# Kernel tuning notes

Measured on AMD Instinct MI355X. Metric: run time of the kernel, lower is better.

The kernel has to match this reference:

```python
import jax, jax.numpy as jnp
import numpy as np

D_MODEL = 2048
N_HEADS = 16
HEAD_DIM = D_MODEL // N_HEADS  # 128
MAX_T = 2048
ROPE_BASE = 10000.0


def _rope_tables(head_dim, max_t, base):
    inv = 1.0 / (base ** (np.arange(0, head_dim, 2, dtype=np.float32) / head_dim))
    t = np.arange(max_t, dtype=np.float32)
    fr = np.outer(t, inv)  # (T, head_dim//2)
    return jnp.asarray(np.cos(fr)), jnp.asarray(np.sin(fr))


def setup_inputs() -> dict:
    key = jax.random.key(0)
    k1, k2, k3 = jax.random.split(key, 3)
    B, T = 2, 2048
    x = jax.random.normal(k1, (B, T, D_MODEL), dtype=jnp.float32)
    Wqkv = jax.random.normal(k2, (3 * D_MODEL, D_MODEL), dtype=jnp.float32) * 0.02
    Wout = jax.random.normal(k3, (D_MODEL, D_MODEL), dtype=jnp.float32) * 0.02
    cos, sin = _rope_tables(HEAD_DIM, MAX_T, ROPE_BASE)
    rope_mask = jnp.arange(N_HEADS) < (N_HEADS // 2)  # first 8 heads RoPE, rest NoPE
    return {"x": x, "Wqkv": Wqkv, "Wout": Wout, "cos": cos, "sin": sin, "rope_mask": rope_mask}


def _apply_rope(t, cos, sin):
    # t: (B,H,T,hd); pairs are consecutive elements (x0,x1),(x2,x3),...
    B, H, T, hd = t.shape
    tr = t.reshape(B, H, T, hd // 2, 2)
    c = cos[:T][None, None, :, :]
    s = sin[:T][None, None, :, :]
    re = tr[..., 0] * c - tr[..., 1] * s
    im = tr[..., 0] * s + tr[..., 1] * c
    return jnp.stack([re, im], axis=-1).reshape(B, H, T, hd)


def reference(x, Wqkv, Wout, cos, sin, rope_mask):
    B, T, D = x.shape
    H = rope_mask.shape[0]
    hd = D // H
    qkv = x @ Wqkv.T  # (B,T,3D)
    q, k, v = jnp.split(qkv, 3, axis=-1)
    def heads(a):
        return a.reshape(B, T, H, hd).transpose(0, 2, 1, 3)  # (B,H,T,hd)
    q, k, v = heads(q), heads(k), heads(v)
    m = rope_mask[None, :, None, None]  # broadcast over (B,H,T,hd)
    q = jnp.where(m, _apply_rope(q, cos, sin), q)
    k = jnp.where(m, _apply_rope(k, cos, sin), k)
    scale = 1.0 / jnp.sqrt(jnp.asarray(hd, dtype=q.dtype))
    scores = jnp.einsum('bhtd,bhsd->bhts', q, k) * scale
    causal = jnp.tril(jnp.ones((T, T), dtype=bool))
    scores = jnp.where(causal[None, None], scores, jnp.asarray(-jnp.inf, dtype=scores.dtype))
    p = jax.nn.softmax(scores, axis=-1)
    out = jnp.einsum('bhts,bhsd->bhtd', p, v)
    out = out.transpose(0, 2, 1, 3).reshape(B, T, D)
    return out @ Wout.T
```

## Files before the change

### kernel.cpp

```cpp
#include <hip/hip_runtime.h>
#include <stdint.h>

typedef unsigned short u16;
typedef __attribute__((ext_vector_type(8))) short short8;
typedef __attribute__((ext_vector_type(4))) short s16x4;
typedef __attribute__((ext_vector_type(4))) float f32x4;

__device__ __forceinline__ u16 f2bf(float f) {
  uint32_t x = __float_as_uint(f);
  x += 0x7fff + ((x >> 16) & 1);
  return (u16)(x >> 16);
}
__device__ __forceinline__ float bf2f(u16 u) {
  return __uint_as_float(((uint32_t)u) << 16);
}
__device__ __forceinline__ f32x4 mfma16(short8 a, short8 b, f32x4 c) {
  return __builtin_amdgcn_mfma_f32_16x16x32_bf16(a, b, c, 0, 0, 0);
}
__device__ __forceinline__ f32x4 mfma16k16(s16x4 a, s16x4 b, f32x4 c) {
  return __builtin_amdgcn_mfma_f32_16x16x16bf16_1k(a, b, c, 0, 0, 0);
}
__device__ __forceinline__ void gld16(const u16* g, u16* l) {
  __builtin_amdgcn_global_load_lds(
      (const __attribute__((address_space(1))) unsigned int*)g,
      (__attribute__((address_space(3))) unsigned int*)l, 16, 0, 0);
}
__device__ __forceinline__ float exp2a(float x) {
  float r;
  asm("v_exp_f32 %0, %1" : "=v"(r) : "v"(x));
  return r;
}

__global__ __launch_bounds__(256) void cvt_all(const float* __restrict__ x,
                                               const float* __restrict__ wqkv,
                                               const float* __restrict__ wout,
                                               u16* __restrict__ xb,
                                               u16* __restrict__ wqkvb,
                                               u16* __restrict__ woutb) {
  long i = ((long)blockIdx.x * 256 + threadIdx.x) * 8;
  const float* s;
  u16* d;
  long off;
  if (i < 8388608) {
    s = x; d = xb; off = i;
  } else if (i < 20971520) {
    s = wqkv; d = wqkvb; off = i - 8388608;
  } else {
    s = wout; d = woutb; off = i - 20971520;
  }
  f32x4 a = *(const f32x4*)(s + off);
  f32x4 b = *(const f32x4*)(s + off + 4);
  short8 o;
#pragma unroll
  for (int j = 0; j < 4; j++) {
    o[j] = (short)f2bf(a[j]);
    o[j + 4] = (short)f2bf(b[j]);
  }
  *(short8*)(d + off) = o;
}

template <int EPI>
__global__ __launch_bounds__(256) void gemm_bt(const u16* __restrict__ A,
                                               const u16* __restrict__ B,
                                               int K, void* __restrict__ Cv, int N) {
  __shared__ __align__(16) u16 As[4096];
  __shared__ __align__(16) u16 Bs[4096];
  const int m0 = blockIdx.y * 128, n0 = blockIdx.x * 128;
  const int t = threadIdx.x, w = t >> 6, lane = t & 63;
  const int quad = lane >> 4, l15 = lane & 15;
  const int rb = (w >> 1) * 64, cb = (w & 1) * 64;
  f32x4 acc[4][4] = {};
  const u16* ag = A + (size_t)(m0 + w * 16 + (lane >> 2)) * K + (lane & 3) * 8;
  const u16* bg = B + (size_t)(n0 + w * 16 + (lane >> 2)) * K + (lane & 3) * 8;
  u16* al = As + w * 512 + lane * 8;
  u16* bl = Bs + w * 512 + lane * 8;
  const size_t rowskip = (size_t)64 * K;
  for (int k0 = 0; k0 < K; k0 += 32) {
    __syncthreads();
    gld16(ag, al);
    gld16(ag + rowskip, al + 2048);
    gld16(bg, bl);
    gld16(bg + rowskip, bl + 2048);
    ag += 32;
    bg += 32;
    __syncthreads();
    short8 af[4], bfr[4];
#pragma unroll
    for (int mf = 0; mf < 4; mf++)
      af[mf] = *(const short8*)&As[(rb + mf * 16 + l15) * 32 + quad * 8];
#pragma unroll
    for (int nf = 0; nf < 4; nf++)
      bfr[nf] = *(const short8*)&Bs[(cb + nf * 16 + l15) * 32 + quad * 8];
#pragma unroll
    for (int mf = 0; mf < 4; mf++)
#pragma unroll
      for (int nf = 0; nf < 4; nf++)
        acc[mf][nf] = mfma16(af[mf], bfr[nf], acc[mf][nf]);
  }
  if (EPI == 0) {
    u16* q3 = (u16*)Cv;
    const int which = n0 >> 11;
    if (which == 2) {
#pragma unroll
      for (int mf = 0; mf < 4; mf++)
#pragma unroll
        for (int nf = 0; nf < 4; nf++) {
          int m = m0 + rb + mf * 16 + quad * 4;
          int n = n0 + cb + nf * 16 + l15;
          int dd = n & 2047, hh = dd >> 7, di = dd & 127;
          int bb = m >> 11, tt = m & 2047;
          s16x4 st;
#pragma unroll
          for (int rg = 0; rg < 4; rg++) st[rg] = (short)f2bf(acc[mf][nf][rg]);
          *(s16x4*)(q3 + 16777216 + ((size_t)(bb * 16 + hh) * 128 + di) * 2048 + tt) = st;
        }
    } else {
      const float sc = (which == 0) ? 0.1275174f : 1.0f;
      u16* base = q3 + (size_t)which * 8388608;
#pragma unroll
      for (int mf = 0; mf < 4; mf++)
#pragma unroll
        for (int nf = 0; nf < 4; nf++) {
          int m = m0 + rb + mf * 16 + quad * 4;
          int n = n0 + cb + nf * 16 + l15;
          int dd = n & 2047, hh = dd >> 7, di = dd & 127;
          int bb = m >> 11, tt = m & 2047;
#pragma unroll
          for (int rg = 0; rg < 4; rg++)
            base[((size_t)(bb * 16 + hh) * 2048 + tt + rg) * 128 + di] =
                f2bf(acc[mf][nf][rg] * sc);
        }
    }
  } else {
    float* C = (float*)Cv;
#pragma unroll
    for (int mf = 0; mf < 4; mf++)
#pragma unroll
      for (int nf = 0; nf < 4; nf++)
#pragma unroll
        for (int rg = 0; rg < 4; rg++) {
          int m = m0 + rb + mf * 16 + quad * 4 + rg;
          int n = n0 + cb + nf * 16 + l15;
          C[(size_t)m * N + n] = acc[mf][nf][rg];
        }
  }
}

__global__ __launch_bounds__(256) void rope_k(u16* __restrict__ q, u16* __restrict__ k,
                                              const float* __restrict__ cosT,
                                              const float* __restrict__ sinT) {
  int t = threadIdx.x;
  int row = blockIdx.x * 4 + (t >> 6);
  int i = t & 63;
  int b = row >> 14;
  int h = (row >> 11) & 7;
  int tp = row & 2047;
  size_t base = ((size_t)((b * 16 + h) * 2048 + tp)) * 128 + 2 * i;
  float c = cosT[tp * 64 + i], s = sinT[tp * 64 + i];
  {
    uint32_t u = *(uint32_t*)(q + base);
    float x0 = bf2f((u16)(u & 0xffff)), x1 = bf2f((u16)(u >> 16));
    float re = x0 * c - x1 * s, im = x0 * s + x1 * c;
    *(uint32_t*)(q + base) = (uint32_t)f2bf(re) | ((uint32_t)f2bf(im) << 16);
  }
  {
    uint32_t u = *(uint32_t*)(k + base);
    float x0 = bf2f((u16)(u & 0xffff)), x1 = bf2f((u16)(u >> 16));
    float re = x0 * c - x1 * s, im = x0 * s + x1 * c;
    *(uint32_t*)(k + base) = (uint32_t)f2bf(re) | ((uint32_t)f2bf(im) << 16);
  }
}

__global__ __launch_bounds__(256, 2) void attn_k(const u16* __restrict__ qh,
                                                 const u16* __restrict__ kh,
                                                 const u16* __restrict__ vTh,
                                                 u16* __restrict__ attno) {
  __shared__ __align__(16) u16 Ks[8192];
  __shared__ __align__(16) u16 Vt[8192];
  const int i = blockIdx.x;
  const int jj = i & 255, half = i >> 8;
  const int bh = jj >> 3, t8 = jj & 7;
  const int qt = half ? (15 - t8) : t8;
  const int q0 = qt * 128;
  const int t = threadIdx.x, w = t >> 6, lane = t & 63;
  const int quad = lane >> 4, l15 = lane & 15;
  const size_t bhoff = (size_t)bh * 262144;

  short8 qb[2][4];
  {
    const u16* qp = qh + bhoff + (size_t)(q0 + w * 32 + l15) * 128 + quad * 8;
#pragma unroll
    for (int qq = 0; qq < 2; qq++)
#pragma unroll
      for (int ks = 0; ks < 4; ks++)
        qb[qq][ks] = *(const short8*)(qp + qq * 2048 + ks * 32);
  }
  f32x4 of[2][8] = {};
  float mst[2] = {-1e30f, -1e30f}, lst[2] = {0.f, 0.f};
  const int nkt = 2 * qt + 2;
  const int wq0 = q0 + w * 32;

  for (int kt = 0; kt < nkt; kt++) {
    const int k0 = kt * 64;
    __syncthreads();
    {
#pragma unroll
      for (int it = 0; it < 4; it++) {
        int L = it * 256 + t;
        int key = L >> 4, c = L & 15;
        gld16(kh + bhoff + (size_t)(k0 + key) * 128 + ((c ^ (key & 15)) * 8),
              Ks + (size_t)L * 8);
      }
#pragma unroll
      for (int it = 0; it < 4; it++) {
        int L = it * 256 + t;
        int d = L >> 3, c = L & 7;
        gld16(vTh + bhoff + (size_t)d * 2048 + k0 + ((c ^ (d & 7)) * 8),
              Vt + (size_t)L * 8);
      }
    }
    __syncthreads();
    if (k0 <= wq0 + 31) {
      f32x4 sacc[2][4];
#pragma unroll
      for (int qq = 0; qq < 2; qq++)
#pragma unroll
        for (int kk = 0; kk < 4; kk++) sacc[qq][kk] = (f32x4){0.f, 0.f, 0.f, 0.f};
#pragma unroll
      for (int kk = 0; kk < 4; kk++) {
        short8 kf[4];
#pragma unroll
        for (int ks = 0; ks < 4; ks++)
          kf[ks] = *(const short8*)&Ks[(kk * 16 + l15) * 128 + ((ks * 4 + quad) ^ l15) * 8];
#pragma unroll
        for (int qq = 0; qq < 2; qq++)
#pragma unroll
          for (int ks = 0; ks < 4; ks++)
            sacc[qq][kk] = mfma16(kf[ks], qb[qq][ks], sacc[qq][kk]);
      }
      const bool needmask = (k0 + 63 > wq0);
      s16x4 pf[2][4];
      float alpha[2];
#pragma unroll
      for (int qq = 0; qq < 2; qq++) {
        const int qg = wq0 + qq * 16 + l15;
        if (needmask) {
#pragma unroll
          for (int kk = 0; kk < 4; kk++)
#pragma unroll
            for (int rg = 0; rg < 4; rg++)
              if (k0 + kk * 16 + quad * 4 + rg > qg) sacc[qq][kk][rg] = -1e30f;
        }
        float pm = -1e30f;
#pragma unroll
        for (int kk = 0; kk < 4; kk++)
#pragma unroll
          for (int rg = 0; rg < 4; rg++) pm = fmaxf(pm, sacc[qq][kk][rg]);
        pm = fmaxf(pm, __shfl_xor(pm, 16));
        pm = fmaxf(pm, __shfl_xor(pm, 32));
        float mnew = fmaxf(mst[qq], pm);
        alpha[qq] = exp2a(mst[qq] - mnew);
        mst[qq] = mnew;
        float ps = 0.f;
#pragma unroll
        for (int kk = 0; kk < 4; kk++) {
          float e0 = exp2a(sacc[qq][kk][0] - mnew);
          float e1 = exp2a(sacc[qq][kk][1] - mnew);
          float e2 = exp2a(sacc[qq][kk][2] - mnew);
          float e3 = exp2a(sacc[qq][kk][3] - mnew);
          ps += (e0 + e1) + (e2 + e3);
          pf[qq][kk][0] = (short)f2bf(e0);
          pf[qq][kk][1] = (short)f2bf(e1);
          pf[qq][kk][2] = (short)f2bf(e2);
          pf[qq][kk][3] = (short)f2bf(e3);
        }
        ps += __shfl_xor(ps, 16);
        ps += __shfl_xor(ps, 32);
        lst[qq] = lst[qq] * alpha[qq] + ps;
      }
#pragma unroll
      for (int qq = 0; qq < 2; qq++) {
        if (!__all(alpha[qq] == 1.0f)) {
          float a = alpha[qq];
#pragma unroll
          for (int df = 0; df < 8; df++) of[qq][df] *= a;
        }
      }
#pragma unroll
      for (int df = 0; df < 8; df++) {
        s16x4 vf[4];
#pragma unroll
        for (int kk = 0; kk < 4; kk++)
          vf[kk] = *(const s16x4*)&Vt[(df * 16 + l15) * 64 +
                                      ((kk * 2 + (quad >> 1)) ^ (l15 & 7)) * 8 +
                                      (quad & 1) * 4];
#pragma unroll
        for (int qq = 0; qq < 2; qq++)
#pragma unroll
          for (int kk = 0; kk < 4; kk++)
            of[qq][df] = mfma16k16(vf[kk], pf[qq][kk], of[qq][df]);
      }
    }
  }
  const int b = bh >> 4, h = bh & 15;
#pragma unroll
  for (int qq = 0; qq < 2; qq++) {
    float linv = 1.0f / lst[qq];
    const size_t row = (size_t)(b * 2048 + q0 + w * 32 + qq * 16 + l15);
#pragma unroll
    for (int df = 0; df < 8; df++) {
      s16x4 o;
#pragma unroll
      for (int rg = 0; rg < 4; rg++) o[rg] = (short)f2bf(of[qq][df][rg] * linv);
      *(s16x4*)(attno + row * 2048 + h * 128 + df * 16 + quad * 4) = o;
    }
  }
}

extern "C" void kernel_launch(void* const* d_in, const int* in_sizes, int n_in,
                              void* d_out, int out_size, void* d_ws, size_t ws_size,
                              hipStream_t stream) {
  const float* x = (const float*)d_in[0];
  const float* Wqkv = (const float*)d_in[1];
  const float* Wout = (const float*)d_in[2];
  const float* cosT = (const float*)d_in[3];
  const float* sinT = (const float*)d_in[4];
  float* out = (float*)d_out;
  char* ws = (char*)d_ws;
  u16* qkvh = (u16*)(ws + 0);
  u16* woutb = (u16*)(ws + 50331648);
  u16* xb = (u16*)(ws + 58720256);
  u16* wqkvb = (u16*)(ws + 75497472);
  u16* attno = wqkvb;

  cvt_all<<<12288, 256, 0, stream>>>(x, Wqkv, Wout, xb, wqkvb, woutb);
  gemm_bt<0><<<dim3(48, 32), 256, 0, stream>>>(xb, wqkvb, 2048, (void*)qkvh, 0);
  rope_k<<<8192, 256, 0, stream>>>(qkvh, qkvh + 8388608, cosT, sinT);
  attn_k<<<512, 256, 0, stream>>>(qkvh, qkvh + 8388608, qkvh + 16777216, attno);
  gemm_bt<1><<<dim3(16, 32), 256, 0, stream>>>(attno, woutb, 2048, (void*)out, 2048);
}
```

Measured before the change: 418.7 us.

## Fuse RoPE into QKV GEMM epilogue and stage outputs through LDS

The QKV projection epilogue now writes its accumulator tile to shared memory and then emits coalesced vector stores. It applies the RoPE rotation and the query scale in the same pass for the rotated heads. This removes the separate rope kernel and its read-modify-write of Q and K. The output-projection GEMM uses the same LDS-staged epilogue for coalesced float4 stores. In exchange the epilogue adds extra barriers and LDS traffic per fragment row.

```diff
diff --git a/kernel.cpp b/kernel.cpp
--- a/kernel.cpp
+++ b/kernel.cpp
@@ -62,9 +62,12 @@
 template <int EPI>
 __global__ __launch_bounds__(256) void gemm_bt(const u16* __restrict__ A,
                                                const u16* __restrict__ B,
-                                               int K, void* __restrict__ Cv, int N) {
-  __shared__ __align__(16) u16 As[4096];
-  __shared__ __align__(16) u16 Bs[4096];
+                                               int K, void* __restrict__ Cv, int N,
+                                               const float* __restrict__ cosT,
+                                               const float* __restrict__ sinT) {
+  __shared__ __align__(16) u16 SMEM[8448];
+  u16* As = SMEM;
+  u16* Bs = SMEM + 4096;
   const int m0 = blockIdx.y * 128, n0 = blockIdx.x * 128;
   const int t = threadIdx.x, w = t >> 6, lane = t & 63;
   const int quad = lane >> 4, l15 = lane & 15;
@@ -97,77 +100,76 @@
       for (int nf = 0; nf < 4; nf++)
         acc[mf][nf] = mfma16(af[mf], bfr[nf], acc[mf][nf]);
   }
-  if (EPI == 0) {
-    u16* q3 = (u16*)Cv;
-    const int which = n0 >> 11;
-    if (which == 2) {
-#pragma unroll
-      for (int mf = 0; mf < 4; mf++)
-#pragma unroll
-        for (int nf = 0; nf < 4; nf++) {
-          int m = m0 + rb + mf * 16 + quad * 4;
-          int n = n0 + cb + nf * 16 + l15;
-          int dd = n & 2047, hh = dd >> 7, di = dd & 127;
-          int bb = m >> 11, tt = m & 2047;
-          s16x4 st;
-#pragma unroll
-          for (int rg = 0; rg < 4; rg++) st[rg] = (short)f2bf(acc[mf][nf][rg]);
-          *(s16x4*)(q3 + 16777216 + ((size_t)(bb * 16 + hh) * 128 + di) * 2048 + tt) = st;
-        }
+
+  float* Es = (float*)SMEM;
+  const int tt0m = m0 & 2047;
+  const int bb = m0 >> 11;
+  const int lr0 = (w >> 1) * 16 + quad * 4;
+#pragma unroll
+  for (int mf = 0; mf < 4; mf++) {
+    __syncthreads();
+#pragma unroll
+    for (int nf = 0; nf < 4; nf++) {
+      const int col = cb + nf * 16 + l15;
+#pragma unroll
+      for (int rg = 0; rg < 4; rg++) Es[(lr0 + rg) * 132 + col] = acc[mf][nf][rg];
+    }
+    __syncthreads();
+    if (EPI == 1) {
+      float* C = (float*)Cv;
+#pragma unroll
+      for (int it = 0; it < 4; it++) {
+        int idx = it * 256 + t;
+        int row = idx >> 5, ch = idx & 31;
+        int ri = (row < 16) ? (mf * 16 + row) : (64 + mf * 16 + row - 16);
+        f32x4 vv = *(const f32x4*)&Es[row * 132 + ch * 4];
+        *(f32x4*)&C[(size_t)(m0 + ri) * N + n0 + ch * 4] = vv;
+      }
     } else {
-      const float sc = (which == 0) ? 0.1275174f : 1.0f;
-      u16* base = q3 + (size_t)which * 8388608;
-#pragma unroll
-      for (int mf = 0; mf < 4; mf++)
-#pragma unroll
-        for (int nf = 0; nf < 4; nf++) {
-          int m = m0 + rb + mf * 16 + quad * 4;
-          int n = n0 + cb + nf * 16 + l15;
-          int dd = n & 2047, hh = dd >> 7, di = dd & 127;
-          int bb = m >> 11, tt = m & 2047;
-#pragma unroll
-          for (int rg = 0; rg < 4; rg++)
-            base[((size_t)(bb * 16 + hh) * 2048 + tt + rg) * 128 + di] =
-                f2bf(acc[mf][nf][rg] * sc);
-        }
-    }
-  } else {
-    float* C = (float*)Cv;
-#pragma unroll
-    for (int mf = 0; mf < 4; mf++)
-#pragma unroll
-      for (int nf = 0; nf < 4; nf++)
-#pragma unroll
-        for (int rg = 0; rg < 4; rg++) {
-          int m = m0 + rb + mf * 16 + quad * 4 + rg;
-          int n = n0 + cb + nf * 16 + l15;
-          C[(size_t)m * N + n] = acc[mf][nf][rg];
-        }
-  }
-}
-
-__global__ __launch_bounds__(256) void rope_k(u16* __restrict__ q, u16* __restrict__ k,
-                                              const float* __restrict__ cosT,
-                                              const float* __restrict__ sinT) {
-  int t = threadIdx.x;
-  int row = blockIdx.x * 4 + (t >> 6);
-  int i = t & 63;
-  int b = row >> 14;
-  int h = (row >> 11) & 7;
-  int tp = row & 2047;
-  size_t base = ((size_t)((b * 16 + h) * 2048 + tp)) * 128 + 2 * i;
-  float c = cosT[tp * 64 + i], s = sinT[tp * 64 + i];
-  {
-    uint32_t u = *(uint32_t*)(q + base);
-    float x0 = bf2f((u16)(u & 0xffff)), x1 = bf2f((u16)(u >> 16));
-    float re = x0 * c - x1 * s, im = x0 * s + x1 * c;
-    *(uint32_t*)(q + base) = (uint32_t)f2bf(re) | ((uint32_t)f2bf(im) << 16);
-  }
-  {
-    uint32_t u = *(uint32_t*)(k + base);
-    float x0 = bf2f((u16)(u & 0xffff)), x1 = bf2f((u16)(u >> 16));
-    float re = x0 * c - x1 * s, im = x0 * s + x1 * c;
-    *(uint32_t*)(k + base) = (uint32_t)f2bf(re) | ((uint32_t)f2bf(im) << 16);
+      const int which = n0 >> 11;
+      const int hh = (n0 & 2047) >> 7;
+      u16* q3 = (u16*)Cv;
+      if (which == 2) {
+        u16* vbase = q3 + 16777216 + ((size_t)(bb * 16 + hh) * 128) * 2048;
+#pragma unroll
+        for (int it = 0; it < 2; it++) {
+          int idx = it * 256 + t;
+          int di = idx & 127, rc = idx >> 7;
+          int r0 = rc * 8;
+          int tb = tt0m + ((r0 < 16) ? (mf * 16 + r0) : (64 + mf * 16 + r0 - 16));
+          short8 o;
+#pragma unroll
+          for (int j = 0; j < 8; j++) o[j] = (short)f2bf(Es[(r0 + j) * 132 + di]);
+          *(short8*)(vbase + (size_t)di * 2048 + tb) = o;
+        }
+      } else {
+        const float sc = (which == 0) ? 0.1275174f : 1.0f;
+        const bool doRope = (hh < 8);
+        u16* base = q3 + (size_t)which * 8388608 + ((size_t)(bb * 16 + hh) * 2048) * 128;
+#pragma unroll
+        for (int it = 0; it < 4; it++) {
+          int idx = it * 256 + t;
+          int row = idx >> 5, ch = idx & 31;
+          int ri = (row < 16) ? (mf * 16 + row) : (64 + mf * 16 + row - 16);
+          int tt = tt0m + ri;
+          f32x4 vv = *(const f32x4*)&Es[row * 132 + ch * 4];
+          vv *= sc;
+          if (doRope) {
+            float2 cc = *(const float2*)&cosT[(size_t)tt * 64 + ch * 2];
+            float2 ss = *(const float2*)&sinT[(size_t)tt * 64 + ch * 2];
+            float r0 = vv[0] * cc.x - vv[1] * ss.x;
+            float i0 = vv[0] * ss.x + vv[1] * cc.x;
+            float r1 = vv[2] * cc.y - vv[3] * ss.y;
+            float i1 = vv[2] * ss.y + vv[3] * cc.y;
+            vv[0] = r0; vv[1] = i0; vv[2] = r1; vv[3] = i1;
+          }
+          s16x4 o;
+#pragma unroll
+          for (int j = 0; j < 4; j++) o[j] = (short)f2bf(vv[j]);
+          *(s16x4*)(base + (size_t)tt * 128 + ch * 4) = o;
+        }
+      }
+    }
   }
 }
 
@@ -334,8 +336,9 @@
   u16* attno = wqkvb;
 
   cvt_all<<<12288, 256, 0, stream>>>(x, Wqkv, Wout, xb, wqkvb, woutb);
-  gemm_bt<0><<<dim3(48, 32), 256, 0, stream>>>(xb, wqkvb, 2048, (void*)qkvh, 0);
-  rope_k<<<8192, 256, 0, stream>>>(qkvh, qkvh + 8388608, cosT, sinT);
+  gemm_bt<0><<<dim3(48, 32), 256, 0, stream>>>(xb, wqkvb, 2048, (void*)qkvh, 0,
+                                               cosT, sinT);
   attn_k<<<512, 256, 0, stream>>>(qkvh, qkvh + 8388608, qkvh + 16777216, attno);
-  gemm_bt<1><<<dim3(16, 32), 256, 0, stream>>>(attno, woutb, 2048, (void*)out, 2048);
-}
+  gemm_bt<1><<<dim3(16, 32), 256, 0, stream>>>(attno, woutb, 2048, (void*)out, 2048,
+                                               nullptr, nullptr);
+}
```

Result: slower. 429.5 us (+2.6%).

## Switch GEMM to 32x32x16 MFMA and stage fp32 output through LDS

Applied to the files above, without the earlier changes.

Replaces the 16x16x32 MFMA tiling in the projection GEMM with 32x32x16 MFMAs (2x2 fragments per wave), cutting LDS fragment loads per MFMA flop and the MFMA issue count. The epilogues are rewritten for the new accumulator layout. The fp32 output projection now stages each 32-row slab through shared memory so it can write coalesced 16-byte rows instead of scattered scalar stores. This costs extra LDS traffic and barriers in the epilogue.

```diff
diff --git a/kernel.cpp b/kernel.cpp
--- a/kernel.cpp
+++ b/kernel.cpp
@@ -5,6 +5,7 @@
 typedef __attribute__((ext_vector_type(8))) short short8;
 typedef __attribute__((ext_vector_type(4))) short s16x4;
 typedef __attribute__((ext_vector_type(4))) float f32x4;
+typedef __attribute__((ext_vector_type(16))) float f32x16;
 
 __device__ __forceinline__ u16 f2bf(float f) {
   uint32_t x = __float_as_uint(f);
@@ -16,6 +17,9 @@
 }
 __device__ __forceinline__ f32x4 mfma16(short8 a, short8 b, f32x4 c) {
   return __builtin_amdgcn_mfma_f32_16x16x32_bf16(a, b, c, 0, 0, 0);
+}
+__device__ __forceinline__ f32x16 mfma32(short8 a, short8 b, f32x16 c) {
+  return __builtin_amdgcn_mfma_f32_32x32x16_bf16(a, b, c, 0, 0, 0);
 }
 __device__ __forceinline__ f32x4 mfma16k16(s16x4 a, s16x4 b, f32x4 c) {
   return __builtin_amdgcn_mfma_f32_16x16x16bf16_1k(a, b, c, 0, 0, 0);
@@ -63,13 +67,14 @@
 __global__ __launch_bounds__(256) void gemm_bt(const u16* __restrict__ A,
                                                const u16* __restrict__ B,
                                                int K, void* __restrict__ Cv, int N) {
-  __shared__ __align__(16) u16 As[4096];
-  __shared__ __align__(16) u16 Bs[4096];
+  __shared__ __align__(16) u16 SMEM[8448];
+  u16* As = SMEM;
+  u16* Bs = SMEM + 4096;
   const int m0 = blockIdx.y * 128, n0 = blockIdx.x * 128;
   const int t = threadIdx.x, w = t >> 6, lane = t & 63;
-  const int quad = lane >> 4, l15 = lane & 15;
+  const int l31 = lane & 31, half = lane >> 5;
   const int rb = (w >> 1) * 64, cb = (w & 1) * 64;
-  f32x4 acc[4][4] = {};
+  f32x16 acc[2][2] = {};
   const u16* ag = A + (size_t)(m0 + w * 16 + (lane >> 2)) * K + (lane & 3) * 8;
   const u16* bg = B + (size_t)(n0 + w * 16 + (lane >> 2)) * K + (lane & 3) * 8;
   u16* al = As + w * 512 + lane * 8;
@@ -84,65 +89,90 @@
     ag += 32;
     bg += 32;
     __syncthreads();
-    short8 af[4], bfr[4];
-#pragma unroll
-    for (int mf = 0; mf < 4; mf++)
-      af[mf] = *(const short8*)&As[(rb + mf * 16 + l15) * 32 + quad * 8];
-#pragma unroll
-    for (int nf = 0; nf < 4; nf++)
-      bfr[nf] = *(const short8*)&Bs[(cb + nf * 16 + l15) * 32 + quad * 8];
-#pragma unroll
-    for (int mf = 0; mf < 4; mf++)
-#pragma unroll
-      for (int nf = 0; nf < 4; nf++)
-        acc[mf][nf] = mfma16(af[mf], bfr[nf], acc[mf][nf]);
-  }
+    short8 af[2][2], bfr[2][2];
+#pragma unroll
+    for (int mi = 0; mi < 2; mi++)
+#pragma unroll
+      for (int kh = 0; kh < 2; kh++)
+        af[mi][kh] = *(const short8*)&As[(rb + mi * 32 + l31) * 32 + kh * 16 + half * 8];
+#pragma unroll
+    for (int ni = 0; ni < 2; ni++)
+#pragma unroll
+      for (int kh = 0; kh < 2; kh++)
+        bfr[ni][kh] = *(const short8*)&Bs[(cb + ni * 32 + l31) * 32 + kh * 16 + half * 8];
+#pragma unroll
+    for (int kh = 0; kh < 2; kh++)
+#pragma unroll
+      for (int mi = 0; mi < 2; mi++)
+#pragma unroll
+        for (int ni = 0; ni < 2; ni++)
+          acc[mi][ni] = mfma32(af[mi][kh], bfr[ni][kh], acc[mi][ni]);
+  }
+
   if (EPI == 0) {
+    const int which = n0 >> 11;
+    const int hh = (n0 & 2047) >> 7;
+    const int bb = m0 >> 11, tt0 = m0 & 2047;
     u16* q3 = (u16*)Cv;
-    const int which = n0 >> 11;
     if (which == 2) {
-#pragma unroll
-      for (int mf = 0; mf < 4; mf++)
-#pragma unroll
-        for (int nf = 0; nf < 4; nf++) {
-          int m = m0 + rb + mf * 16 + quad * 4;
-          int n = n0 + cb + nf * 16 + l15;
-          int dd = n & 2047, hh = dd >> 7, di = dd & 127;
-          int bb = m >> 11, tt = m & 2047;
-          s16x4 st;
-#pragma unroll
-          for (int rg = 0; rg < 4; rg++) st[rg] = (short)f2bf(acc[mf][nf][rg]);
-          *(s16x4*)(q3 + 16777216 + ((size_t)(bb * 16 + hh) * 128 + di) * 2048 + tt) = st;
+      u16* vbase = q3 + 16777216 + ((size_t)(bb * 16 + hh) * 128) * 2048;
+#pragma unroll
+      for (int mi = 0; mi < 2; mi++)
+#pragma unroll
+        for (int ni = 0; ni < 2; ni++) {
+          int di = cb + ni * 32 + l31;
+          int trow = tt0 + rb + mi * 32 + half * 4;
+#pragma unroll
+          for (int rg2 = 0; rg2 < 4; rg2++) {
+            s16x4 st;
+#pragma unroll
+            for (int j = 0; j < 4; j++) st[j] = (short)f2bf(acc[mi][ni][rg2 * 4 + j]);
+            *(s16x4*)(vbase + (size_t)di * 2048 + trow + rg2 * 8) = st;
+          }
         }
     } else {
       const float sc = (which == 0) ? 0.1275174f : 1.0f;
-      u16* base = q3 + (size_t)which * 8388608;
-#pragma unroll
-      for (int mf = 0; mf < 4; mf++)
-#pragma unroll
-        for (int nf = 0; nf < 4; nf++) {
-          int m = m0 + rb + mf * 16 + quad * 4;
-          int n = n0 + cb + nf * 16 + l15;
-          int dd = n & 2047, hh = dd >> 7, di = dd & 127;
-          int bb = m >> 11, tt = m & 2047;
-#pragma unroll
-          for (int rg = 0; rg < 4; rg++)
-            base[((size_t)(bb * 16 + hh) * 2048 + tt + rg) * 128 + di] =
-                f2bf(acc[mf][nf][rg] * sc);
+      u16* base = q3 + (size_t)which * 8388608 + ((size_t)(bb * 16 + hh) * 2048) * 128;
+#pragma unroll
+      for (int mi = 0; mi < 2; mi++)
+#pragma unroll
+        for (int ni = 0; ni < 2; ni++) {
+          int di = cb + ni * 32 + l31;
+          int trow = tt0 + rb + mi * 32 + half * 4;
+#pragma unroll
+          for (int reg = 0; reg < 16; reg++) {
+            int tt = trow + (reg & 3) + 8 * (reg >> 2);
+            base[(size_t)tt * 128 + di] = f2bf(acc[mi][ni][reg] * sc);
+          }
         }
     }
   } else {
+    float* Es = (float*)SMEM;
     float* C = (float*)Cv;
 #pragma unroll
-    for (int mf = 0; mf < 4; mf++)
-#pragma unroll
-      for (int nf = 0; nf < 4; nf++)
-#pragma unroll
-        for (int rg = 0; rg < 4; rg++) {
-          int m = m0 + rb + mf * 16 + quad * 4 + rg;
-          int n = n0 + cb + nf * 16 + l15;
-          C[(size_t)m * N + n] = acc[mf][nf][rg];
-        }
+    for (int r = 0; r < 4; r++) {
+      __syncthreads();
+      if ((w >> 1) == (r >> 1)) {
+        const int mi = r & 1;
+#pragma unroll
+        for (int ni = 0; ni < 2; ni++) {
+          int col = cb + ni * 32 + l31;
+#pragma unroll
+          for (int reg = 0; reg < 16; reg++) {
+            int lrow = (reg & 3) + 8 * (reg >> 2) + half * 4;
+            Es[lrow * 132 + col] = acc[mi][ni][reg];
+          }
+        }
+      }
+      __syncthreads();
+#pragma unroll
+      for (int it = 0; it < 4; it++) {
+        int idx = it * 256 + t;
+        int row = idx >> 5, ch = idx & 31;
+        f32x4 vv = *(const f32x4*)&Es[row * 132 + ch * 4];
+        *(f32x4*)&C[(size_t)(m0 + r * 32 + row) * N + n0 + ch * 4] = vv;
+      }
+    }
   }
 }
 
```

Result: no change. 419.0 us (+0.1%).
